# Kernel tuning notes

Hardware: AMD Instinct MI355X
Metric: run time of the kernel (lower is better)

The kernel has to match this reference:

```python
import jax, jax.numpy as jnp
import numpy as np

SPAN = 20
REPEAT = 90


def setup_inputs() -> dict:
    key = jax.random.key(0)
    k1, k2 = jax.random.split(key)
    B, C, H, W = 4, 1, 512, 512
    pred = jax.random.normal(k1, (B, C, H, W), dtype=jnp.float32)
    gt = jax.random.normal(k2, (B, C, H, W), dtype=jnp.float32)
    # random offsets: magnitude in [1, span], random sign (matches np.random logic in torch module)
    rng = np.random.default_rng(0)
    mag_h = rng.integers(1, SPAN + 1, size=REPEAT)
    mag_w = rng.integers(1, SPAN + 1, size=REPEAT)
    sign_h = np.where(rng.uniform(size=REPEAT) > 0.5, -1, 1)
    sign_w = np.where(rng.uniform(size=REPEAT) > 0.5, -1, 1)
    h_offsets = jnp.asarray(mag_h * sign_h, dtype=jnp.int32)
    w_offsets = jnp.asarray(mag_w * sign_w, dtype=jnp.int32)
    return {"pred": pred, "gt": gt, "h_offsets": h_offsets, "w_offsets": w_offsets}


def _relative_depth(x, h_offsets, w_offsets):
    """x: [B,C,H,W] -> [B,Hb,Wb,R*C] stack of base-block minus shifted-block diffs."""
    B, C, H, W = x.shape
    Hb, Wb = H - 2 * SPAN, W - 2 * SPAN
    base = jax.lax.dynamic_slice(x, (0, 0, SPAN, SPAN), (B, C, Hb, Wb))

    def one_shift(h, w):
        shifted = jax.lax.dynamic_slice(x, (0, 0, SPAN + h, SPAN + w), (B, C, Hb, Wb))
        return base - shifted

    rd = jax.vmap(one_shift)(h_offsets, w_offsets)          # [R,B,C,Hb,Wb]
    R = rd.shape[0]
    rd = jnp.transpose(rd, (1, 0, 2, 3, 4)).reshape(B, R * C, Hb, Wb)  # concat along channel
    return jnp.transpose(rd, (0, 2, 3, 1))                   # [B,Hb,Wb,R*C]


def _l2_normalize(rd):
    norm = jnp.linalg.norm(rd, axis=-1, keepdims=True)
    norm = jnp.where(norm == 0, jnp.ones_like(norm), norm)
    return rd / norm


def reference(pred, gt, h_offsets, w_offsets):
    pred_rd = _l2_normalize(_relative_depth(pred, h_offsets, w_offsets))
    gt_rd = _l2_normalize(_relative_depth(gt, h_offsets, w_offsets))
    return jnp.mean(jnp.abs(pred_rd - gt_rd))
```

## Files before the change

kernel.cpp:

```cpp
#include <hip/hip_runtime.h>
#include <hip/hip_fp16.h>

#define SPAN 20
#define REPEAT 90


constexpr int W  = 512;
constexpr int Wb = 472;
constexpr int TJ = 64;
constexpr int TI = 8;
constexpr int TW = TJ + 2 * SPAN;
constexpr int TH = TI + 2 * SPAN;
constexpr int QW = TW / 2;
constexpr int PLANE = TH * QW;

typedef unsigned int u32;

static __device__ __forceinline__ u32 packpg(float p, float g) {
    const __half2 h = __floats2half2_rn(p, g);
    return __builtin_bit_cast(u32, h);
}
static __device__ __forceinline__ __half2 h2(u32 v) {
    return __builtin_bit_cast(__half2, v);
}

__global__ __launch_bounds__(256, 4) void rd_loss_kernel(
    const float* __restrict__ pred, const float* __restrict__ gt,
    const int* __restrict__ hoff, const int* __restrict__ woff,
    float* __restrict__ out)
{
    __shared__ uint2 plane[2][PLANE];
    __shared__ float wsum[4];

    const int t  = threadIdx.x;
    const int bx = blockIdx.x;
    const int by = blockIdx.y;
    const int b  = blockIdx.z;
    const int I0 = by * TI;
    const int J0 = bx * TJ;

    const float* pb_ = pred + b * (W * W);
    const float* gb_ = gt   + b * (W * W);

    for (int e = t; e < PLANE; e += 256) {
        const int row = e / QW;
        const int q   = e - row * QW;
        const int gr  = I0 + row;
        int c0 = J0 + 2 * q;  c0 = c0 < 510 ? c0 : 510;
        int c2 = c0 + 2;      c2 = c2 < 510 ? c2 : 510;
        const float2 pLo = *(const float2*)(pb_ + gr * W + c0);
        const float2 gLo = *(const float2*)(gb_ + gr * W + c0);
        const float2 pHi = *(const float2*)(pb_ + gr * W + c2);
        const float2 gHi = *(const float2*)(gb_ + gr * W + c2);
        const u32 h0 = packpg(pLo.x, gLo.x);
        const u32 h1 = packpg(pLo.y, gLo.y);
        const u32 hx = packpg(pHi.x, gHi.x);
        plane[0][e] = make_uint2(h0, h1);
        plane[1][e] = make_uint2(h1, hx);
    }
    __syncthreads();

    const int jp  = t & 31;
    const int row = t >> 5;
    const bool ok0 = (J0 + 2 * jp)     < Wb;
    const bool ok1 = (J0 + 2 * jp + 1) < Wb;

    const int lanebase = row * QW + jp;
    const uint2 cc = plane[0][(SPAN + row) * QW + (SPAN / 2 + jp)];
    const __half2 c0 = h2(cc.x), c1 = h2(cc.y);

    __half2 sA0 = __floats2half2_rn(0.f, 0.f), sB0 = sA0;
    __half2 sA1 = sA0, sB1 = sA0;
    #pragma unroll
    for (int r = 0; r < REPEAT; ++r) {
        const int ho = hoff[r], wo = woff[r];
        const int pi = wo & 1;
        const int uo = (SPAN + ho) * QW + ((SPAN + wo - pi) >> 1);
        const uint2 vv = plane[pi][lanebase + uo];
        const __half2 d0 = __hsub2(c0, h2(vv.x));
        const __half2 d1 = __hsub2(c1, h2(vv.y));
        if (r & 1) { sB0 = __hfma2(d0, d0, sB0); sB1 = __hfma2(d1, d1, sB1); }
        else       { sA0 = __hfma2(d0, d0, sA0); sA1 = __hfma2(d1, d1, sA1); }
    }

    asm volatile("" ::: "memory");

    const float ssp0 = __half2float(__low2half(sA0))  + __half2float(__low2half(sB0));
    const float ssg0 = __half2float(__high2half(sA0)) + __half2float(__high2half(sB0));
    const float ssp1 = __half2float(__low2half(sA1))  + __half2float(__low2half(sB1));
    const float ssg1 = __half2float(__high2half(sA1)) + __half2float(__high2half(sB1));

    const float invp0 = (ssp0 == 0.f) ? 1.f : rsqrtf(ssp0);
    const float invg0 = (ssg0 == 0.f) ? 1.f : rsqrtf(ssg0);
    const float invp1 = (ssp1 == 0.f) ? 1.f : rsqrtf(ssp1);
    const float invg1 = (ssg1 == 0.f) ? 1.f : rsqrtf(ssg1);

    const __half nr0 = __float2half(-(invg0 / invp0));
    const __half nr1 = __float2half(-(invg1 / invp1));

    __half a0A = __float2half(0.f), a0B = a0A, a1A = a0A, a1B = a0A;
    #pragma unroll
    for (int r = 0; r < REPEAT; ++r) {
        const int ho = hoff[r], wo = woff[r];
        const int pi = wo & 1;
        const int uo = (SPAN + ho) * QW + ((SPAN + wo - pi) >> 1);
        const uint2 vv = plane[pi][lanebase + uo];
        const __half2 d0 = __hsub2(c0, h2(vv.x));
        const __half2 d1 = __hsub2(c1, h2(vv.y));
        const __half s0 = __hfma(nr0, __high2half(d0), __low2half(d0));
        const __half s1 = __hfma(nr1, __high2half(d1), __low2half(d1));
        if (r & 1) { a0B = __hadd(a0B, __habs(s0)); a1B = __hadd(a1B, __habs(s1)); }
        else       { a0A = __hadd(a0A, __habs(s0)); a1A = __hadd(a1A, __habs(s1)); }
    }
    const float l0 = invp0 * (__half2float(a0A) + __half2float(a0B));
    const float l1 = invp1 * (__half2float(a1A) + __half2float(a1B));

    float lsum = (ok0 ? l0 : 0.f) + (ok1 ? l1 : 0.f);

    #pragma unroll
    for (int o = 32; o > 0; o >>= 1) lsum += __shfl_down(lsum, o, 64);

    const int lane = t & 63;
    const int wid  = t >> 6;
    if (lane == 0) wsum[wid] = lsum;
    __syncthreads();

    if (t == 0) {
        const float s = wsum[0] + wsum[1] + wsum[2] + wsum[3];
        constexpr float scale = 1.0f / (4.0f * 472.0f * 472.0f * 90.0f);
        atomicAdd(out, s * scale);
    }
}

extern "C" void kernel_launch(void* const* d_in, const int* in_sizes, int n_in,
                              void* d_out, int out_size, void* d_ws, size_t ws_size,
                              hipStream_t stream) {
    const float* pred = (const float*)d_in[0];
    const float* gt   = (const float*)d_in[1];
    const int* hoff   = (const int*)d_in[2];
    const int* woff   = (const int*)d_in[3];
    float* out = (float*)d_out;

    hipMemsetAsync(out, 0, sizeof(float), stream);

    dim3 grid(8, 59, 4);
    rd_loss_kernel<<<grid, 256, 0, stream>>>(pred, gt, hoff, woff, out);
}
```

Before: 51.90 us.

## Replace dual parity LDS planes with single packed tile and raise occupancy bound

Drops the two parity-shifted shared-memory planes in favour of one packed half2 (pred,gt) tile, halving LDS footprint and the staging loads and stores. Each shift now does two 32-bit LDS reads at an arbitrary column offset instead of one aligned 64-bit read. The launch bound's blocks-per-CU hint is raised from 4 to 8 to allow more resident blocks. The trade-off is twice the LDS read instructions in both inner loops, possible bank-conflict changes, and a tighter register budget.

```diff
diff --git a/kernel.cpp b/kernel.cpp
--- a/kernel.cpp
+++ b/kernel.cpp
@@ -12,24 +12,23 @@
 constexpr int TW = TJ + 2 * SPAN;
 constexpr int TH = TI + 2 * SPAN;
 constexpr int QW = TW / 2;
-constexpr int PLANE = TH * QW;
+constexpr int NPAIR = TH * QW;
 
 typedef unsigned int u32;
 
 static __device__ __forceinline__ u32 packpg(float p, float g) {
-    const __half2 h = __floats2half2_rn(p, g);
-    return __builtin_bit_cast(u32, h);
+    return __builtin_bit_cast(u32, __floats2half2_rn(p, g));
 }
 static __device__ __forceinline__ __half2 h2(u32 v) {
     return __builtin_bit_cast(__half2, v);
 }
 
-__global__ __launch_bounds__(256, 4) void rd_loss_kernel(
+__global__ __launch_bounds__(256, 8) void rd_loss_kernel(
     const float* __restrict__ pred, const float* __restrict__ gt,
     const int* __restrict__ hoff, const int* __restrict__ woff,
     float* __restrict__ out)
 {
-    __shared__ uint2 plane[2][PLANE];
+    __shared__ u32 tile[TH * TW];
     __shared__ float wsum[4];
 
     const int t  = threadIdx.x;
@@ -42,21 +41,15 @@
     const float* pb_ = pred + b * (W * W);
     const float* gb_ = gt   + b * (W * W);
 
-    for (int e = t; e < PLANE; e += 256) {
+    for (int e = t; e < NPAIR; e += 256) {
         const int row = e / QW;
         const int q   = e - row * QW;
         const int gr  = I0 + row;
-        int c0 = J0 + 2 * q;  c0 = c0 < 510 ? c0 : 510;
-        int c2 = c0 + 2;      c2 = c2 < 510 ? c2 : 510;
-        const float2 pLo = *(const float2*)(pb_ + gr * W + c0);
-        const float2 gLo = *(const float2*)(gb_ + gr * W + c0);
-        const float2 pHi = *(const float2*)(pb_ + gr * W + c2);
-        const float2 gHi = *(const float2*)(gb_ + gr * W + c2);
-        const u32 h0 = packpg(pLo.x, gLo.x);
-        const u32 h1 = packpg(pLo.y, gLo.y);
-        const u32 hx = packpg(pHi.x, gHi.x);
-        plane[0][e] = make_uint2(h0, h1);
-        plane[1][e] = make_uint2(h1, hx);
+        int gc = J0 + 2 * q; gc = gc < 510 ? gc : 510;
+        const float2 pv = *(const float2*)(pb_ + gr * W + gc);
+        const float2 gv = *(const float2*)(gb_ + gr * W + gc);
+        *(uint2*)&tile[2 * e] = make_uint2(packpg(pv.x, gv.x),
+                                           packpg(pv.y, gv.y));
     }
     __syncthreads();
 
@@ -65,20 +58,20 @@
     const bool ok0 = (J0 + 2 * jp)     < Wb;
     const bool ok1 = (J0 + 2 * jp + 1) < Wb;
 
-    const int lanebase = row * QW + jp;
-    const uint2 cc = plane[0][(SPAN + row) * QW + (SPAN / 2 + jp)];
-    const __half2 c0 = h2(cc.x), c1 = h2(cc.y);
+    const int cbase = (SPAN + row) * TW + (SPAN + 2 * jp);
+    const __half2 c0 = h2(tile[cbase]);
+    const __half2 c1 = h2(tile[cbase + 1]);
 
     __half2 sA0 = __floats2half2_rn(0.f, 0.f), sB0 = sA0;
     __half2 sA1 = sA0, sB1 = sA0;
     #pragma unroll
     for (int r = 0; r < REPEAT; ++r) {
-        const int ho = hoff[r], wo = woff[r];
-        const int pi = wo & 1;
-        const int uo = (SPAN + ho) * QW + ((SPAN + wo - pi) >> 1);
-        const uint2 vv = plane[pi][lanebase + uo];
-        const __half2 d0 = __hsub2(c0, h2(vv.x));
-        const __half2 d1 = __hsub2(c1, h2(vv.y));
+        const int off = hoff[r] * TW + woff[r];
+        const int a   = cbase + off;
+        const u32 v0 = tile[a];
+        const u32 v1 = tile[a + 1];
+        const __half2 d0 = __hsub2(c0, h2(v0));
+        const __half2 d1 = __hsub2(c1, h2(v1));
         if (r & 1) { sB0 = __hfma2(d0, d0, sB0); sB1 = __hfma2(d1, d1, sB1); }
         else       { sA0 = __hfma2(d0, d0, sA0); sA1 = __hfma2(d1, d1, sA1); }
     }
@@ -101,12 +94,12 @@
     __half a0A = __float2half(0.f), a0B = a0A, a1A = a0A, a1B = a0A;
     #pragma unroll
     for (int r = 0; r < REPEAT; ++r) {
-        const int ho = hoff[r], wo = woff[r];
-        const int pi = wo & 1;
-        const int uo = (SPAN + ho) * QW + ((SPAN + wo - pi) >> 1);
-        const uint2 vv = plane[pi][lanebase + uo];
-        const __half2 d0 = __hsub2(c0, h2(vv.x));
-        const __half2 d1 = __hsub2(c1, h2(vv.y));
+        const int off = hoff[r] * TW + woff[r];
+        const int a   = cbase + off;
+        const u32 v0 = tile[a];
+        const u32 v1 = tile[a + 1];
+        const __half2 d0 = __hsub2(c0, h2(v0));
+        const __half2 d1 = __hsub2(c1, h2(v1));
         const __half s0 = __hfma(nr0, __high2half(d0), __low2half(d0));
         const __half s1 = __hfma(nr1, __high2half(d1), __low2half(d1));
         if (r & 1) { a0B = __hadd(a0B, __habs(s0)); a1B = __hadd(a1B, __habs(s1)); }
```

Result: no change. 50.95 us (-1.8%).
